# Kernel optimization log

Hardware: AMD Instinct MI355X
Metric: run time of the kernel (lower is better)

The kernel has to match this reference:

```python
import jax, jax.numpy as jnp
import numpy as np

K = 3            # kernel_size
PAD = (K - 1) // 2
UM = 2           # um_dim
C_IN = 128
C_OUT = 128
SLOPE = 0.01     # F.leaky_relu default negative slope


def setup_inputs() -> dict:
    key = jax.random.key(0)
    k1, k2, k3 = jax.random.split(key, 3)
    xx = jax.random.normal(k1, (16, C_IN, 64, 64), dtype=jnp.float32)
    # Conv2d(C_in, C_out, K, stride=K, bias=True) parameters
    w = jax.random.normal(k2, (C_OUT, C_IN, K, K), dtype=jnp.float32) * 0.05
    b = jax.random.normal(k3, (C_OUT,), dtype=jnp.float32) * 0.05
    return {"xx": xx, "w": w, "b": b}


def reference(xx, w, b):
    B, C, H, Wd = xx.shape
    # --- unfold: replicate pad, then extract all KxK patches (stride 1) ---
    xp = jnp.pad(xx, ((0, 0), (0, 0), (PAD, PAD), (PAD, PAD)), mode="edge")
    # patches[b, c, r, s, i, j] = xp[b, c, i + r, j + s]   -> [B, C, K, K, H, W]
    patches = jnp.stack(
        [jnp.stack([xp[:, :, r:r + H, s:s + Wd] for s in range(K)], axis=2)
         for r in range(K)], axis=2)
    # --- subtract per-(um-slot, pixel) mean over channel groups and KxK ---
    g = patches.reshape(B, C // UM, UM, K, K, H, Wd)
    avgs = g.mean(axis=(1, 3, 4), keepdims=True)        # [B,1,UM,1,1,H,W]
    g = g - avgs
    p = g.reshape(B, C, K, K, H, Wd)
    # --- patch-wise conv (kernel_size == stride on the tiled image). The
    # torch code's transpose(2,4).transpose(-1,-2) tiling places patch col
    # offset s along tiled rows and row offset r along tiled cols, so the
    # conv weight w[o,c,r,s] pairs with patches[b,c,s,r,i,j]. ---
    out = jnp.einsum("ocrs,bcsrij->boij", w, p) + b[None, :, None, None]
    # leaky_relu
    out = jnp.where(out > 0, out, SLOPE * out)
    # --- add mean back per um-slot ---
    m = avgs[:, :, :, 0, 0]                             # [B,1,UM,H,W]
    O = out.shape[1]
    out = out.reshape(B, O // UM, UM, H, Wd) + m
    return out.reshape(B, O, H, Wd)
```

## Files before the change

### kernel.cpp

```cpp
#include <hip/hip_runtime.h>
#include <hip/hip_bf16.h>

typedef __bf16 bf16x8 __attribute__((ext_vector_type(8)));
typedef float  f32x4  __attribute__((ext_vector_type(4)));

#define NB 16
#define CI 128
#define CO 128
#define HH 64
#define WW 64

#define SROWS 4
#define SCOLS 66
#define SSTR  72

__global__ void prep(const float* __restrict__ w, __bf16* __restrict__ Ag,
                     float* __restrict__ wsum) {
    __shared__ float red[8];
    const int blk = blockIdx.x, tid = threadIdx.x;
    if (blk < 72) {
        int gid  = blk * 256 + tid;
        int l    = gid & 63;
        int frag = gid >> 6;
        int mt   = frag & 7;
        int t    = frag >> 3;
        int tap  = t >> 2;
        int r    = tap % 3;
        int s    = tap / 3;
        int o    = mt * 16 + (l & 15);
        int cb   = (t & 3) * 32 + (l >> 4) * 8;
        bf16x8 v;
        #pragma unroll
        for (int j = 0; j < 8; ++j)
            v[j] = (__bf16)w[((o * CI + cb + j) * 3 + r) * 3 + s];
        *(bf16x8*)(Ag + (size_t)gid * 8) = v;
    } else {
        int o = blk - 72;
        const float* p = w + (size_t)o * CI * 9;
        float se = 0.f, so = 0.f;
        for (int idx = tid; idx < CI * 9; idx += 256) {
            int c = idx / 9;
            float v = p[idx];
            if (c & 1) so += v; else se += v;
        }
        #pragma unroll
        for (int off = 32; off; off >>= 1) {
            se += __shfl_down(se, off);
            so += __shfl_down(so, off);
        }
        int wave = tid >> 6, lane = tid & 63;
        if (lane == 0) { red[wave * 2] = se; red[wave * 2 + 1] = so; }
        __syncthreads();
        if (tid == 0) {
            wsum[o]      = red[0] + red[2] + red[4] + red[6];
            wsum[CO + o] = red[1] + red[3] + red[5] + red[7];
        }
    }
}

__global__ __launch_bounds__(512, 4) void conv_main(
        const float* __restrict__ x,
        const float* __restrict__ bias,
        const float* __restrict__ wsum,
        const __bf16* __restrict__ Ag,
        float* __restrict__ out)
{
    __shared__ __align__(16) __bf16 slab[SROWS * SCOLS * SSTR];
    __shared__ float Srow[SROWS * SCOLS * 2];
    __shared__ float avgl[2 * 64 * 2];

    const int tid  = threadIdx.x;
    const int b    = blockIdx.y;
    const int row0 = blockIdx.x * 2;

    const float* xb = x + (size_t)b * CI * HH * WW;

    const int wave = tid >> 6, lane = tid & 63;
    const int wm = wave >> 2;
    const int wn = wave & 3;
    const int rsel = wn >> 1, csel = wn & 1;
    const int m = lane & 15, q = lane >> 4;

    f32x4 acc[4][2];
    #pragma unroll
    for (int i = 0; i < 4; ++i)
        #pragma unroll
        for (int j = 0; j < 2; ++j)
            acc[i][j] = (f32x4){0.f, 0.f, 0.f, 0.f};

    int bbase[2];
    #pragma unroll
    for (int nt = 0; nt < 2; ++nt)
        bbase[nt] = (rsel * SCOLS + csel * 32 + nt * 16 + m) * SSTR + q * 8;

    const __bf16* Abase = Ag + ((size_t)(wm * 4) << 9) + ((size_t)lane << 3);

    for (int half = 0; half < 2; ++half) {
        const int t0 = half * 2;
        bf16x8 Acur[4];
        #pragma unroll
        for (int i = 0; i < 4; ++i)
            Acur[i] = *(const bf16x8*)(Abase + (t0 << 12) + (i << 9));

        if (half) __syncthreads();
        for (int u = tid; u < SROWS * SCOLS * 8; u += 512) {
            int col = u % SCOLS;
            int rc  = u / SCOLS;
            int cg  = rc & 7;
            int r   = rc >> 3;
            int yi  = row0 - 1 + r; yi = yi < 0 ? 0 : (yi > HH - 1 ? HH - 1 : yi);
            int xi  = col - 1;      xi = xi < 0 ? 0 : (xi > WW - 1 ? WW - 1 : xi);
            const float* src = xb + (size_t)(half * 64 + cg * 8) * (HH * WW)
                                  + yi * WW + xi;
            bf16x8 v;
            #pragma unroll
            for (int j = 0; j < 8; ++j)
                v[j] = (__bf16)src[(size_t)j * (HH * WW)];
            *(bf16x8*)(slab + (r * SCOLS + col) * SSTR + cg * 8) = v;
        }
        __syncthreads();
        for (int u = tid; u < SROWS * SCOLS; u += 512) {
            const __bf16* p = slab + u * SSTR;
            float se = 0.f, so = 0.f;
            #pragma unroll
            for (int cg = 0; cg < 8; ++cg) {
                bf16x8 v = *(const bf16x8*)(p + cg * 8);
                se += (float)v[0] + (float)v[2] + (float)v[4] + (float)v[6];
                so += (float)v[1] + (float)v[3] + (float)v[5] + (float)v[7];
            }
            if (half) { se += Srow[u * 2 + 0]; so += Srow[u * 2 + 1]; }
            Srow[u * 2 + 0] = se;
            Srow[u * 2 + 1] = so;
        }
        __syncthreads();
        if (half == 1) {
            if (tid < 256) {
                int uu  = tid & 1;
                int col = (tid >> 1) & 63;
                int rr  = tid >> 7;
                float ssum = 0.f;
                #pragma unroll
                for (int dy = 0; dy < 3; ++dy)
                    #pragma unroll
                    for (int dx = 0; dx < 3; ++dx)
                        ssum += Srow[(((rr + dy) * SCOLS) + (col + dx)) * 2 + uu];
                avgl[tid] = ssum * (1.0f / 576.0f);
            }
            __syncthreads();
        }
        for (int it = 0; it < 18; ++it) {
            int itn  = it + 1 < 18 ? it + 1 : it;
            int tn   = (itn >> 1) * 4 + half * 2 + (itn & 1);
            bf16x8 Anx[4];
            #pragma unroll
            for (int i = 0; i < 4; ++i)
                Anx[i] = *(const bf16x8*)(Abase + (tn << 12) + (i << 9));
            int tap = it >> 1, cc = it & 1;
            int s_  = tap >= 6 ? 2 : (tap >= 3 ? 1 : 0);
            int r3  = tap - s_ * 3;
            int boff = (s_ * SCOLS + r3) * SSTR + cc * 32;
            bf16x8 Bf[2];
            #pragma unroll
            for (int nt = 0; nt < 2; ++nt)
                Bf[nt] = *(const bf16x8*)(slab + bbase[nt] + boff);
            #pragma unroll
            for (int i = 0; i < 4; ++i)
                #pragma unroll
                for (int nt = 0; nt < 2; ++nt)
                    acc[i][nt] = __builtin_amdgcn_mfma_f32_16x16x32_bf16(
                        Acur[i], Bf[nt], acc[i][nt], 0, 0, 0);
            #pragma unroll
            for (int i = 0; i < 4; ++i)
                Acur[i] = Anx[i];
        }
    }

    float a0v[2], a1v[2];
    #pragma unroll
    for (int nt = 0; nt < 2; ++nt) {
        int col = csel * 32 + nt * 16 + m;
        a0v[nt] = avgl[rsel * 128 + col * 2 + 0];
        a1v[nt] = avgl[rsel * 128 + col * 2 + 1];
    }
    float* outb = out + (size_t)b * CO * HH * WW + (size_t)(row0 + rsel) * WW
                      + csel * 32;
    #pragma unroll
    for (int i = 0; i < 4; ++i) {
        #pragma unroll
        for (int rg = 0; rg < 4; ++rg) {
            int o = wm * 64 + i * 16 + q * 4 + rg;
            float bo = bias[o];
            float w0 = wsum[o];
            float w1 = wsum[CO + o];
            float* po = outb + (size_t)o * (HH * WW);
            #pragma unroll
            for (int nt = 0; nt < 2; ++nt) {
                float v = acc[i][nt][rg] + bo - a0v[nt] * w0 - a1v[nt] * w1;
                v = v > 0.f ? v : 0.01f * v;
                v += (o & 1) ? a1v[nt] : a0v[nt];
                __builtin_nontemporal_store(v, po + nt * 16 + m);
            }
        }
    }
}

extern "C" void kernel_launch(void* const* d_in, const int* in_sizes, int n_in,
                              void* d_out, int out_size, void* d_ws, size_t ws_size,
                              hipStream_t stream) {
    const float* x    = (const float*)d_in[0];
    const float* w    = (const float*)d_in[1];
    const float* bias = (const float*)d_in[2];
    float* out = (float*)d_out;

    __bf16* Ag   = (__bf16*)d_ws;
    float*  wsum = (float*)((char*)d_ws + 294912);

    prep<<<200, 256, 0, stream>>>(w, Ag, wsum);

    dim3 grid(HH / 2, NB);
    conv_main<<<grid, 512, 0, stream>>>(x, bias, wsum, Ag, out);
}
```

Baseline: 112.7 us.

## Pre-transpose input to channel-last bf16 and double-buffer slab over channel quarters

A new prep pass transposes x from NCHW fp32 into four channel-quarter buffers of NHWC bf16. The conv kernel can then fill its shared-memory slab with contiguous 16-byte loads instead of eight strided scalar loads per element. The main loop now walks four 32-channel quarters with a double-buffered slab, register-staged prefetch of the next quarter, and the channel sums folded into the loop. The cost is an extra pass over the input through global memory plus a second launch. The prep kernel also carries a dead Ag-writing branch that never runs with 1024 blocks.

```diff
diff --git a/kernel.cpp b/kernel.cpp
--- a/kernel.cpp
+++ b/kernel.cpp
@@ -12,10 +12,59 @@
 
 #define SROWS 4
 #define SCOLS 66
-#define SSTR  72
-
-__global__ void prep(const float* __restrict__ w, __bf16* __restrict__ Ag,
-                     float* __restrict__ wsum) {
+#define SSTR  40
+#define QSZ   ((size_t)16 * 64 * 64 * 32)
+
+__global__ void prep(const float* __restrict__ x, __bf16* __restrict__ Ag,
+                     float* __restrict__ wsum, __bf16* __restrict__ xT) {
+    __shared__ float tile[128 * 65];
+    const int blk = blockIdx.x, tid = threadIdx.x;
+    if (blk < 1024) {
+        const int bb = blk >> 6, y = blk & 63;
+        const float* xr = x + ((size_t)bb * CI) * (HH * WW) + y * WW;
+        for (int idx = tid; idx < 2048; idx += 256) {
+            int c = idx >> 4, x4 = idx & 15;
+            float4 v = *(const float4*)(xr + (size_t)c * (HH * WW) + x4 * 4);
+            *(float4*)(tile + c * 65 + x4 * 4) = v;
+        }
+        __syncthreads();
+        for (int idx = tid; idx < 1024; idx += 256) {
+            int px = idx >> 4, cg = idx & 15;
+            bf16x8 o8;
+            #pragma unroll
+            for (int j = 0; j < 8; ++j)
+                o8[j] = (__bf16)tile[(cg * 8 + j) * 65 + px];
+            __bf16* dst = xT + (size_t)(cg >> 2) * QSZ
+                        + (((size_t)bb * 64 + y) * 64 + px) * 32 + (cg & 3) * 8;
+            *(bf16x8*)dst = o8;
+        }
+    } else if (blk < 1096) {
+        int gid  = (blk - 1024) * 256 + tid;
+        int l    = gid & 63;
+        int frag = gid >> 6;
+        int mt   = frag & 7;
+        int t    = frag >> 3;
+        int tap  = t >> 2;
+        int r    = tap % 3;
+        int s    = tap / 3;
+        int o    = mt * 16 + (l & 15);
+        int cb   = (t & 3) * 32 + (l >> 4) * 8;
+        bf16x8 v;
+        #pragma unroll
+        for (int j = 0; j < 8; ++j)
+            v[j] = (__bf16)x[0];
+        #pragma unroll
+        for (int j = 0; j < 8; ++j) {
+            v[j] = (__bf16)((const float*)wsum == nullptr ? 0.f : 0.f);
+        }
+        const float* w = (const float*)xT;
+        (void)w;
+        *(bf16x8*)(Ag + (size_t)gid * 8) = v;
+    }
+}
+
+__global__ void prep_w(const float* __restrict__ w, __bf16* __restrict__ Ag,
+                       float* __restrict__ wsum) {
     __shared__ float red[8];
     const int blk = blockIdx.x, tid = threadIdx.x;
     if (blk < 72) {
@@ -59,27 +108,25 @@
 }
 
 __global__ __launch_bounds__(512, 4) void conv_main(
-        const float* __restrict__ x,
+        const __bf16* __restrict__ xT,
         const float* __restrict__ bias,
         const float* __restrict__ wsum,
         const __bf16* __restrict__ Ag,
         float* __restrict__ out)
 {
-    __shared__ __align__(16) __bf16 slab[SROWS * SCOLS * SSTR];
+    __shared__ __align__(16) __bf16 slab[2][SROWS * SCOLS * SSTR];
     __shared__ float Srow[SROWS * SCOLS * 2];
-    __shared__ float avgl[2 * 64 * 2];
+    __shared__ float avgl[256];
 
     const int tid  = threadIdx.x;
     const int b    = blockIdx.y;
     const int row0 = blockIdx.x * 2;
-
-    const float* xb = x + (size_t)b * CI * HH * WW;
 
     const int wave = tid >> 6, lane = tid & 63;
     const int wm = wave >> 2;
     const int wn = wave & 3;
     const int rsel = wn >> 1, csel = wn & 1;
-    const int m = lane & 15, q = lane >> 4;
+    const int m = lane & 15, qv = lane >> 4;
 
     f32x4 acc[4][2];
     #pragma unroll
@@ -91,78 +138,74 @@
     int bbase[2];
     #pragma unroll
     for (int nt = 0; nt < 2; ++nt)
-        bbase[nt] = (rsel * SCOLS + csel * 32 + nt * 16 + m) * SSTR + q * 8;
+        bbase[nt] = (rsel * SCOLS + csel * 32 + nt * 16 + m) * SSTR + qv * 8;
 
     const __bf16* Abase = Ag + ((size_t)(wm * 4) << 9) + ((size_t)lane << 3);
 
-    for (int half = 0; half < 2; ++half) {
-        const int t0 = half * 2;
-        bf16x8 Acur[4];
-        #pragma unroll
-        for (int i = 0; i < 4; ++i)
-            Acur[i] = *(const bf16x8*)(Abase + (t0 << 12) + (i << 9));
-
-        if (half) __syncthreads();
-        for (int u = tid; u < SROWS * SCOLS * 8; u += 512) {
-            int col = u % SCOLS;
-            int rc  = u / SCOLS;
-            int cg  = rc & 7;
-            int r   = rc >> 3;
-            int yi  = row0 - 1 + r; yi = yi < 0 ? 0 : (yi > HH - 1 ? HH - 1 : yi);
-            int xi  = col - 1;      xi = xi < 0 ? 0 : (xi > WW - 1 ? WW - 1 : xi);
-            const float* src = xb + (size_t)(half * 64 + cg * 8) * (HH * WW)
-                                  + yi * WW + xi;
-            bf16x8 v;
-            #pragma unroll
-            for (int j = 0; j < 8; ++j)
-                v[j] = (__bf16)src[(size_t)j * (HH * WW)];
-            *(bf16x8*)(slab + (r * SCOLS + col) * SSTR + cg * 8) = v;
-        }
-        __syncthreads();
-        for (int u = tid; u < SROWS * SCOLS; u += 512) {
-            const __bf16* p = slab + u * SSTR;
-            float se = 0.f, so = 0.f;
-            #pragma unroll
-            for (int cg = 0; cg < 8; ++cg) {
-                bf16x8 v = *(const bf16x8*)(p + cg * 8);
-                se += (float)v[0] + (float)v[2] + (float)v[4] + (float)v[6];
-                so += (float)v[1] + (float)v[3] + (float)v[5] + (float)v[7];
+    bf16x8 sreg[3];
+    auto stage_load = [&](int qq) {
+        #pragma unroll
+        for (int k = 0; k < 3; ++k) {
+            int u  = tid + (k << 9);
+            int uc = u < 1056 ? u : 1055;
+            int cg = uc & 3, pc = uc >> 2;
+            int col = pc % 66, r = pc / 66;
+            int yi = row0 - 1 + r; yi = yi < 0 ? 0 : (yi > HH - 1 ? HH - 1 : yi);
+            int xi = col - 1;      xi = xi < 0 ? 0 : (xi > WW - 1 ? WW - 1 : xi);
+            sreg[k] = *(const bf16x8*)(xT + (size_t)qq * QSZ
+                        + (((size_t)b * 64 + yi) * 64 + xi) * 32 + cg * 8);
+        }
+    };
+    auto stage_write = [&](int buf) {
+        #pragma unroll
+        for (int k = 0; k < 3; ++k) {
+            int u = tid + (k << 9);
+            if (u < 1056) {
+                int cg = u & 3, pc = u >> 2;
+                *(bf16x8*)(&slab[buf][pc * SSTR + cg * 8]) = sreg[k];
             }
-            if (half) { se += Srow[u * 2 + 0]; so += Srow[u * 2 + 1]; }
-            Srow[u * 2 + 0] = se;
-            Srow[u * 2 + 1] = so;
-        }
-        __syncthreads();
-        if (half == 1) {
-            if (tid < 256) {
-                int uu  = tid & 1;
-                int col = (tid >> 1) & 63;
-                int rr  = tid >> 7;
-                float ssum = 0.f;
-                #pragma unroll
-                for (int dy = 0; dy < 3; ++dy)
+        }
+    };
+
+    bf16x8 Acur[4];
+    #pragma unroll
+    for (int i = 0; i < 4; ++i)
+        Acur[i] = *(const bf16x8*)(Abase + ((size_t)i << 9));
+    stage_load(0);
+    stage_write(0);
+    __syncthreads();
+
+    for (int qq = 0; qq < 4; ++qq) {
+        const __bf16* sl = slab[qq & 1];
+        #pragma unroll
+        for (int tap = 0; tap < 9; ++tap) {
+            int tn = (tap < 8) ? ((tap + 1) * 4 + qq) : (qq < 3 ? qq + 1 : 35);
+            bf16x8 Anx[4];
+            #pragma unroll
+            for (int i = 0; i < 4; ++i)
+                Anx[i] = *(const bf16x8*)(Abase + ((size_t)(tn * 8 + i) << 9));
+            if (tap == 0) {
+                if (qq < 3) stage_load(qq + 1);
+                if (tid < SROWS * SCOLS) {
+                    const __bf16* p = sl + tid * SSTR;
+                    float se = 0.f, so = 0.f;
                     #pragma unroll
-                    for (int dx = 0; dx < 3; ++dx)
-                        ssum += Srow[(((rr + dy) * SCOLS) + (col + dx)) * 2 + uu];
-                avgl[tid] = ssum * (1.0f / 576.0f);
+                    for (int cg = 0; cg < 4; ++cg) {
+                        bf16x8 v = *(const bf16x8*)(p + cg * 8);
+                        se += (float)v[0] + (float)v[2] + (float)v[4] + (float)v[6];
+                        so += (float)v[1] + (float)v[3] + (float)v[5] + (float)v[7];
+                    }
+                    if (qq == 0) { Srow[tid * 2] = se;  Srow[tid * 2 + 1] = so; }
+                    else         { Srow[tid * 2] += se; Srow[tid * 2 + 1] += so; }
+                }
             }
-            __syncthreads();
-        }
-        for (int it = 0; it < 18; ++it) {
-            int itn  = it + 1 < 18 ? it + 1 : it;
-            int tn   = (itn >> 1) * 4 + half * 2 + (itn & 1);
-            bf16x8 Anx[4];
-            #pragma unroll
-            for (int i = 0; i < 4; ++i)
-                Anx[i] = *(const bf16x8*)(Abase + (tn << 12) + (i << 9));
-            int tap = it >> 1, cc = it & 1;
-            int s_  = tap >= 6 ? 2 : (tap >= 3 ? 1 : 0);
-            int r3  = tap - s_ * 3;
-            int boff = (s_ * SCOLS + r3) * SSTR + cc * 32;
+            const int s_ = tap >= 6 ? 2 : (tap >= 3 ? 1 : 0);
+            const int r3 = tap - s_ * 3;
+            const int boff = (s_ * SCOLS + r3) * SSTR;
             bf16x8 Bf[2];
             #pragma unroll
             for (int nt = 0; nt < 2; ++nt)
-                Bf[nt] = *(const bf16x8*)(slab + bbase[nt] + boff);
+                Bf[nt] = *(const bf16x8*)(sl + bbase[nt] + boff);
             #pragma unroll
             for (int i = 0; i < 4; ++i)
                 #pragma unroll
@@ -173,7 +216,26 @@
             for (int i = 0; i < 4; ++i)
                 Acur[i] = Anx[i];
         }
-    }
+        if (qq < 3) {
+            stage_write((qq + 1) & 1);
+            __syncthreads();
+        }
+    }
+
+    __syncthreads();
+    if (tid < 256) {
+        int uu  = tid & 1;
+        int col = (tid >> 1) & 63;
+        int rr  = tid >> 7;
+        float ssum = 0.f;
+        #pragma unroll
+        for (int dy = 0; dy < 3; ++dy)
+            #pragma unroll
+            for (int dx = 0; dx < 3; ++dx)
+                ssum += Srow[(((rr + dy) * SCOLS) + (col + dx)) * 2 + uu];
+        avgl[tid] = ssum * (1.0f / 576.0f);
+    }
+    __syncthreads();
 
     float a0v[2], a1v[2];
     #pragma unroll
@@ -188,7 +250,7 @@
     for (int i = 0; i < 4; ++i) {
         #pragma unroll
         for (int rg = 0; rg < 4; ++rg) {
-            int o = wm * 64 + i * 16 + q * 4 + rg;
+            int o = wm * 64 + i * 16 + qv * 4 + rg;
             float bo = bias[o];
             float w0 = wsum[o];
             float w1 = wsum[CO + o];
@@ -214,9 +276,11 @@
 
     __bf16* Ag   = (__bf16*)d_ws;
     float*  wsum = (float*)((char*)d_ws + 294912);
-
-    prep<<<200, 256, 0, stream>>>(w, Ag, wsum);
+    __bf16* xT   = (__bf16*)((char*)d_ws + 295936);
+
+    prep<<<1024, 256, 0, stream>>>(x, Ag, wsum, xT);
+    prep_w<<<200, 256, 0, stream>>>(w, Ag, wsum);
 
     dim3 grid(HH / 2, NB);
-    conv_main<<<grid, 512, 0, stream>>>(x, bias, wsum, Ag, out);
-}
+    conv_main<<<grid, 512, 0, stream>>>(xT, bias, wsum, Ag, out);
+}
```

New measurement: 132.0 us. +17.1%, slower.
